# Kernel optimization log

Hardware: AMD Instinct MI355X
Metric: run time of the kernel (lower is better)

Reference implementation:

```python
import jax, jax.numpy as jnp
import numpy as np

B, N, F, D, H = 4, 2048, 128, 64, 4
NEG = -1000000000.0


def setup_inputs() -> dict:
    key = jax.random.key(0)
    k1, k2, k3, k4 = jax.random.split(key, 4)
    X = jax.random.normal(k1, (B, N, F), dtype=jnp.float32)
    A = jax.random.randint(k2, (N, N), 0, 2, dtype=jnp.int32)
    kernels = jax.random.normal(k3, (H, F, D), dtype=jnp.float32) * 0.1
    attn_kernels = jax.random.normal(k4, (H, D), dtype=jnp.float32) * 0.1
    return {"X": X, "A": A, "kernels": kernels, "attn_kernels": attn_kernels}


def reference(X, A, kernels, attn_kernels):
    # h: per-head linear projection  [H,B,N,D]
    h = jnp.einsum('bnf,hfd->hbnd', X, kernels)
    # per-node scalar scores e_i = h @ a  [H,B,N]
    s = jnp.einsum('hbnd,hd->hbn', h, attn_kernels)
    # pairwise additive score e_ij = relu(s_i + s_j)  [H,B,N,N]
    e = jax.nn.relu(s[:, :, :, None] + s[:, :, None, :])
    e = jnp.where(A[None, None, :, :] > 0, e, NEG)
    alpha = jax.nn.softmax(e, axis=-1)
    # dropout is identity at inference
    h_prime = jnp.einsum('hbnm,hbmd->hbnd', alpha, h)
    out = jnp.mean(h_prime, axis=0)           # mean over heads -> [B,N,D]
    return jax.nn.leaky_relu(out, negative_slope=0.2)
```

## Files before the change

### kernel.cpp

```cpp
#include <hip/hip_runtime.h>
#include <hip/hip_bf16.h>

typedef __attribute__((ext_vector_type(8))) short short8;
typedef __attribute__((ext_vector_type(4))) float f32x4;
typedef unsigned short u16;
typedef unsigned int u32;

constexpr int CB = 4, CN = 2048, CF = 128, CD = 64, CH = 4;
constexpr int IT = 32;

__device__ inline u32 fmap(float f) {
    u32 b = __float_as_uint(f);
    return b ^ ((u32)(((int)b) >> 31) | 0x80000000u);
}
__device__ inline float funmap(u32 u) {
    u32 b = (u & 0x80000000u) ? (u ^ 0x80000000u) : ~u;
    return __uint_as_float(b);
}
__device__ inline u16 bf16bits(float v) {
    __hip_bfloat16 b = __float2bfloat16(v);
    return *reinterpret_cast<u16*>(&b);
}

__global__ __launch_bounds__(256) void prep_k(const int* __restrict__ A,
                                              const float* __restrict__ W,
                                              u32* __restrict__ mask,
                                              u32* __restrict__ smax_u,
                                              u16* __restrict__ WThi,
                                              u16* __restrict__ WTlo) {
    int blk = blockIdx.x, t = threadIdx.x;
    if (blk < 16384) {
        int gid = blk * 256 + t;
        if (blk == 0 && t < CH * CB) smax_u[t] = 0u;
        unsigned long long mk = __ballot(A[gid] > 0);
        if ((t & 63) == 0) {
            mask[gid >> 5] = (u32)mk;
            mask[(gid >> 5) + 1] = (u32)(mk >> 32);
        }
    } else {
        int idx = (blk - 16384) * 256 + t;
        int h = idx >> 13;
        int f = (idx >> 6) & 127;
        int d = idx & 63;
        float v = W[idx];
        __hip_bfloat16 bh = __float2bfloat16(v);
        float lo = v - __bfloat162float(bh);
        int o = (h * CD + d) * CF + f;
        WThi[o] = *reinterpret_cast<u16*>(&bh);
        WTlo[o] = bf16bits(lo);
    }
}

__global__ __launch_bounds__(256, 2) void proj_k(const float* __restrict__ X,
                                                 const u16* __restrict__ WThi,
                                                 const u16* __restrict__ WTlo,
                                                 const float* __restrict__ AK,
                                                 u16* __restrict__ hT,
                                                 float* __restrict__ sout,
                                                 float* __restrict__ eout,
                                                 u32* __restrict__ smax_u) {
    __shared__ float tr[4][CD][17];

    int blk = blockIdx.x;
    int ntile = blk & 127;
    int b = blk >> 7;
    int n0 = ntile * 16;
    int t = threadIdx.x;
    int w = t >> 6, l = t & 63;
    int h = w;
    int row_l = l & 15, jg = l >> 4;

    const float* xrow = X + ((size_t)b * CN + n0 + row_l) * CF + jg * 8;
    const u16* whi = WThi + (size_t)h * CD * CF;
    const u16* wlo = WTlo + (size_t)h * CD * CF;

    float4 xa[4], xb[4];
#pragma unroll
    for (int kk = 0; kk < 4; ++kk) {
        xa[kk] = *reinterpret_cast<const float4*>(xrow + kk * 32);
        xb[kk] = *reinterpret_cast<const float4*>(xrow + kk * 32 + 4);
    }
    short8 bhi[4][4], blo[4][4];
#pragma unroll
    for (int kk = 0; kk < 4; ++kk)
#pragma unroll
        for (int dt = 0; dt < 4; ++dt) {
            int off = (dt * 16 + row_l) * CF + kk * 32 + jg * 8;
            bhi[kk][dt] = *reinterpret_cast<const short8*>(whi + off);
            blo[kk][dt] = *reinterpret_cast<const short8*>(wlo + off);
        }

    f32x4 c[4];
    f32x4 zero = {0.f, 0.f, 0.f, 0.f};
#pragma unroll
    for (int dt = 0; dt < 4; ++dt) c[dt] = zero;

#pragma unroll
    for (int kk = 0; kk < 4; ++kk) {
        float xv[8] = {xa[kk].x, xa[kk].y, xa[kk].z, xa[kk].w,
                       xb[kk].x, xb[kk].y, xb[kk].z, xb[kk].w};
        short8 ahi, alo;
#pragma unroll
        for (int e = 0; e < 8; ++e) {
            __hip_bfloat16 bh = __float2bfloat16(xv[e]);
            ahi[e] = (short)*reinterpret_cast<u16*>(&bh);
            alo[e] = (short)bf16bits(xv[e] - __bfloat162float(bh));
        }
#pragma unroll
        for (int dt = 0; dt < 4; ++dt) {
            c[dt] = __builtin_amdgcn_mfma_f32_16x16x32_bf16(ahi, bhi[kk][dt], c[dt], 0, 0, 0);
            c[dt] = __builtin_amdgcn_mfma_f32_16x16x32_bf16(ahi, blo[kk][dt], c[dt], 0, 0, 0);
            c[dt] = __builtin_amdgcn_mfma_f32_16x16x32_bf16(alo, bhi[kk][dt], c[dt], 0, 0, 0);
        }
    }

    float av[4];
#pragma unroll
    for (int dt = 0; dt < 4; ++dt) av[dt] = AK[h * CD + dt * 16 + row_l];
    float sacc[4];
#pragma unroll
    for (int r = 0; r < 4; ++r)
        sacc[r] = c[0][r] * av[0] + c[1][r] * av[1] + c[2][r] * av[2] + c[3][r] * av[3];
#pragma unroll
    for (int off = 1; off <= 8; off <<= 1)
#pragma unroll
        for (int r = 0; r < 4; ++r) sacc[r] += __shfl_xor(sacc[r], off, 64);

    float mx = fmaxf(fmaxf(sacc[0], sacc[1]), fmaxf(sacc[2], sacc[3]));
    mx = fmaxf(mx, __shfl_xor(mx, 16, 64));
    mx = fmaxf(mx, __shfl_xor(mx, 32, 64));
    if (l == 0) atomicMax(&smax_u[h * CB + b], fmap(mx));

    if (row_l == 0) {
#pragma unroll
        for (int r = 0; r < 4; ++r) {
            size_t si = (size_t)(h * CB + b) * CN + n0 + jg * 4 + r;
            sout[si] = sacc[r];
            eout[si] = __expf(sacc[r]);
        }
    }

#pragma unroll
    for (int dt = 0; dt < 4; ++dt)
#pragma unroll
        for (int r = 0; r < 4; ++r) tr[w][dt * 16 + row_l][jg * 4 + r] = c[dt][r];
    __syncthreads();

    short8* hTs = reinterpret_cast<short8*>(hT);
    int jc = l >> 5, d0 = l & 31;
#pragma unroll
    for (int half = 0; half < 2; ++half) {
        short8 pk;
#pragma unroll
        for (int e = 0; e < 8; ++e)
            pk[e] = (short)bf16bits(tr[w][half * 32 + d0][jc * 8 + e]);
        hTs[((size_t)(h * CB + b) * 256 + ntile * 2 + jc) * 64 + half * 32 + d0] = pk;
    }
}

__global__ __launch_bounds__(1024, 4) void attn_k(const u16* __restrict__ hT,
                                                  const float* __restrict__ s_ws,
                                                  const float* __restrict__ e_ws,
                                                  const u32* __restrict__ smax_u,
                                                  const u32* __restrict__ mask32,
                                                  float* __restrict__ out) {
    __shared__ alignas(16) float e_sl[CH][CN];
    __shared__ u32 m_lds[IT][65];
    __shared__ float cbuf[CH][2][IT][68];
    __shared__ float lbuf[CH][4][IT];

    int orig = blockIdx.x;
    int xcd = orig & 7, pos = orig >> 3;
    int b = xcd >> 1;
    int it = (xcd & 1) * 32 + pos;
    int i0 = it * IT;
    int t = threadIdx.x, w = t >> 6, l = t & 63;
    int hq = w >> 2, jq = w & 3;
    int row_l = l & 15, jg = l >> 4;

    for (int idx = t; idx < CH * CN; idx += 1024) {
        int hh = idx >> 11, j = idx & 2047;
        e_sl[hh][j] = e_ws[(size_t)(hh * CB + b) * CN + j];
    }
    for (int idx = t; idx < IT * 64; idx += 1024) {
        int r = idx >> 6, wd = idx & 63;
        m_lds[r][wd] = mask32[(size_t)(i0 + r) * 64 + wd];
    }
    __syncthreads();

    float smax = funmap(smax_u[hq * CB + b]);
    float si0 = s_ws[(size_t)(hq * CB + b) * CN + i0 + row_l];
    float si1 = s_ws[(size_t)(hq * CB + b) * CN + i0 + 16 + row_l];
    float m0 = fmaxf(si0 + smax, 0.f), m1 = fmaxf(si1 + smax, 0.f);
    float Ei0 = __expf(si0 - m0), Ci0 = __expf(-m0);
    float Ei1 = __expf(si1 - m1), Ci1 = __expf(-m1);

    f32x4 c0[4], c1[4], cl0, cl1;
    f32x4 zero = {0.f, 0.f, 0.f, 0.f};
#pragma unroll
    for (int dt = 0; dt < 4; ++dt) { c0[dt] = zero; c1[dt] = zero; }
    cl0 = zero; cl1 = zero;

    short8 ones;
#pragma unroll
    for (int e = 0; e < 8; ++e) ones[e] = (short)0x3F80;

    const short8* hp = reinterpret_cast<const short8*>(hT) +
                       ((size_t)(hq * CB + b) * 256 + jq * 64 + jg) * 64 + row_l;

    short8 bfA[4], bfB[4];
#pragma unroll
    for (int dt = 0; dt < 4; ++dt) bfA[dt] = hp[dt * 16];

#define ATTN_STEP(KK, BCUR, BNXT, KNXT)                                          \
    do {                                                                         \
        _Pragma("unroll") for (int dt = 0; dt < 4; ++dt)                         \
            BNXT[dt] = hp[(KNXT) * 256 + dt * 16];                               \
        int jl = jq * 512 + (KK) * 32 + jg * 8;                                  \
        f32x4 ej0 = *reinterpret_cast<const f32x4*>(&e_sl[hq][jl]);              \
        f32x4 ej1 = *reinterpret_cast<const f32x4*>(&e_sl[hq][jl + 4]);          \
        u32 by0 = m_lds[row_l][jq * 16 + (KK)] >> (jg * 8);                      \
        u32 by1 = m_lds[16 + row_l][jq * 16 + (KK)] >> (jg * 8);                 \
        short8 af0, af1;                                                         \
        _Pragma("unroll") for (int e = 0; e < 8; ++e) {                          \
            float ejv = (e < 4) ? ej0[e] : ej1[e - 4];                           \
            float w0 = ((by0 >> e) & 1u) ? fmaxf(Ei0 * ejv, Ci0) : 0.f;          \
            float w1 = ((by1 >> e) & 1u) ? fmaxf(Ei1 * ejv, Ci1) : 0.f;          \
            af0[e] = (short)bf16bits(w0);                                        \
            af1[e] = (short)bf16bits(w1);                                        \
        }                                                                        \
        _Pragma("unroll") for (int dt = 0; dt < 4; ++dt) {                       \
            c0[dt] = __builtin_amdgcn_mfma_f32_16x16x32_bf16(af0, BCUR[dt], c0[dt], 0, 0, 0); \
            c1[dt] = __builtin_amdgcn_mfma_f32_16x16x32_bf16(af1, BCUR[dt], c1[dt], 0, 0, 0); \
        }                                                                        \
        cl0 = __builtin_amdgcn_mfma_f32_16x16x32_bf16(af0, ones, cl0, 0, 0, 0);  \
        cl1 = __builtin_amdgcn_mfma_f32_16x16x32_bf16(af1, ones, cl1, 0, 0, 0);  \
    } while (0)

#pragma unroll
    for (int kp = 0; kp < 8; ++kp) {
        ATTN_STEP(2 * kp, bfA, bfB, 2 * kp + 1);
        ATTN_STEP(2 * kp + 1, bfB, bfA, (2 * kp + 2 < 16) ? 2 * kp + 2 : 15);
    }
#undef ATTN_STEP

    int slot = jq & 1;
    if (row_l == 0)
#pragma unroll
        for (int r = 0; r < 4; ++r) {
            lbuf[hq][jq][jg * 4 + r] = cl0[r];
            lbuf[hq][jq][16 + jg * 4 + r] = cl1[r];
        }
    if (jq < 2) {
#pragma unroll
        for (int dt = 0; dt < 4; ++dt)
#pragma unroll
            for (int r = 0; r < 4; ++r) {
                cbuf[hq][slot][jg * 4 + r][dt * 16 + row_l] = c0[dt][r];
                cbuf[hq][slot][16 + jg * 4 + r][dt * 16 + row_l] = c1[dt][r];
            }
    }
    __syncthreads();
    if (jq >= 2) {
#pragma unroll
        for (int dt = 0; dt < 4; ++dt)
#pragma unroll
            for (int r = 0; r < 4; ++r) {
                cbuf[hq][slot][jg * 4 + r][dt * 16 + row_l] += c0[dt][r];
                cbuf[hq][slot][16 + jg * 4 + r][dt * 16 + row_l] += c1[dt][r];
            }
    }
    __syncthreads();

    for (int idx = t; idx < IT * CD; idx += 1024) {
        int row = idx >> 6, d = idx & 63;
        float acc = 0.f;
#pragma unroll
        for (int h = 0; h < CH; ++h) {
            float num = cbuf[h][0][row][d] + cbuf[h][1][row][d];
            float den = lbuf[h][0][row] + lbuf[h][1][row] + lbuf[h][2][row] + lbuf[h][3][row];
            acc += num / fmaxf(den, 1e-30f);
        }
        float o = acc * 0.25f;
        out[((size_t)b * CN + i0 + row) * CD + d] = o > 0.f ? o : 0.2f * o;
    }
}

extern "C" void kernel_launch(void* const* d_in, const int* in_sizes, int n_in,
                              void* d_out, int out_size, void* d_ws, size_t ws_size,
                              hipStream_t stream) {
    const float* X  = (const float*)d_in[0];
    const int*   A  = (const int*)d_in[1];
    const float* W  = (const float*)d_in[2];
    const float* AK = (const float*)d_in[3];
    float* out = (float*)d_out;

    char* w = (char*)d_ws;
    float* s_ws = (float*)w;    w += 131072;
    float* e_ws = (float*)w;    w += 131072;
    u32* smax_ws = (u32*)w;     w += 256;
    u32* mask_ws = (u32*)w;     w += 524288;
    u16* hT = (u16*)w;          w += 4194304;
    u16* WThi = (u16*)w;        w += 65536;
    u16* WTlo = (u16*)w;        w += 65536;

    prep_k<<<16384 + 128, 256, 0, stream>>>(A, W, mask_ws, smax_ws, WThi, WTlo);
    proj_k<<<CB * (CN / 16), 256, 0, stream>>>(X, WThi, WTlo, AK, hT, s_ws, e_ws, smax_ws);
    attn_k<<<CB * (CN / IT), 1024, 0, stream>>>(hT, s_ws, e_ws, smax_ws, mask_ws, out);
}
```

Before: 68.85 us.

## Pre-swizzle weight fragments for coalesced loads, add MFMA priority, roll attention loop

The prep kernel now writes the bf16 hi/lo weight copies in the exact per-lane MFMA fragment order, so the projection kernel loads each short8 fragment contiguously across lanes instead of with strided gathers. The attention inner step raises wave priority around the MFMA block with s_setprio so matrix work is issued ahead of the other waves' scalar and conversion work. The attention k-loop is changed from fully unrolled to unroll 1, which cuts code size and register pressure but adds loop overhead and may limit cross-iteration scheduling.

```diff
diff --git a/kernel.cpp b/kernel.cpp
--- a/kernel.cpp
+++ b/kernel.cpp
@@ -39,15 +39,17 @@
         }
     } else {
         int idx = (blk - 16384) * 256 + t;
+        int e = idx & 7;
+        int l = (idx >> 3) & 63;
+        int dt = (idx >> 9) & 3;
+        int kk = (idx >> 11) & 3;
         int h = idx >> 13;
-        int f = (idx >> 6) & 127;
-        int d = idx & 63;
-        float v = W[idx];
+        int f = kk * 32 + (l >> 4) * 8 + e;
+        int d = dt * 16 + (l & 15);
+        float v = W[(h * CF + f) * CD + d];
         __hip_bfloat16 bh = __float2bfloat16(v);
-        float lo = v - __bfloat162float(bh);
-        int o = (h * CD + d) * CF + f;
-        WThi[o] = *reinterpret_cast<u16*>(&bh);
-        WTlo[o] = bf16bits(lo);
+        WThi[idx] = *reinterpret_cast<u16*>(&bh);
+        WTlo[idx] = bf16bits(v - __bfloat162float(bh));
     }
 }
 
@@ -71,8 +73,8 @@
     int row_l = l & 15, jg = l >> 4;
 
     const float* xrow = X + ((size_t)b * CN + n0 + row_l) * CF + jg * 8;
-    const u16* whi = WThi + (size_t)h * CD * CF;
-    const u16* wlo = WTlo + (size_t)h * CD * CF;
+    const short8* whiU = reinterpret_cast<const short8*>(WThi) + (size_t)h * 1024 + l;
+    const short8* wloU = reinterpret_cast<const short8*>(WTlo) + (size_t)h * 1024 + l;
 
     float4 xa[4], xb[4];
 #pragma unroll
@@ -85,9 +87,8 @@
     for (int kk = 0; kk < 4; ++kk)
 #pragma unroll
         for (int dt = 0; dt < 4; ++dt) {
-            int off = (dt * 16 + row_l) * CF + kk * 32 + jg * 8;
-            bhi[kk][dt] = *reinterpret_cast<const short8*>(whi + off);
-            blo[kk][dt] = *reinterpret_cast<const short8*>(wlo + off);
+            bhi[kk][dt] = whiU[(kk * 4 + dt) * 64];
+            blo[kk][dt] = wloU[(kk * 4 + dt) * 64];
         }
 
     f32x4 c[4];
@@ -229,18 +230,21 @@
             af0[e] = (short)bf16bits(w0);                                        \
             af1[e] = (short)bf16bits(w1);                                        \
         }                                                                        \
+        __builtin_amdgcn_s_setprio(1);                                           \
         _Pragma("unroll") for (int dt = 0; dt < 4; ++dt) {                       \
             c0[dt] = __builtin_amdgcn_mfma_f32_16x16x32_bf16(af0, BCUR[dt], c0[dt], 0, 0, 0); \
             c1[dt] = __builtin_amdgcn_mfma_f32_16x16x32_bf16(af1, BCUR[dt], c1[dt], 0, 0, 0); \
         }                                                                        \
         cl0 = __builtin_amdgcn_mfma_f32_16x16x32_bf16(af0, ones, cl0, 0, 0, 0);  \
         cl1 = __builtin_amdgcn_mfma_f32_16x16x32_bf16(af1, ones, cl1, 0, 0, 0);  \
+        __builtin_amdgcn_s_setprio(0);                                           \
     } while (0)
 
-#pragma unroll
-    for (int kp = 0; kp < 8; ++kp) {
-        ATTN_STEP(2 * kp, bfA, bfB, 2 * kp + 1);
-        ATTN_STEP(2 * kp + 1, bfB, bfA, (2 * kp + 2 < 16) ? 2 * kp + 2 : 15);
+#pragma unroll 1
+    for (int kp = 0; kp < 16; kp += 2) {
+        ATTN_STEP(kp, bfA, bfB, kp + 1);
+        int kn = (kp + 2 < 16) ? kp + 2 : 15;
+        ATTN_STEP(kp + 1, bfB, bfA, kn);
     }
 #undef ATTN_STEP
 
@@ -295,14 +299,14 @@
     const float* AK = (const float*)d_in[3];
     float* out = (float*)d_out;
 
-    char* w = (char*)d_ws;
-    float* s_ws = (float*)w;    w += 131072;
-    float* e_ws = (float*)w;    w += 131072;
-    u32* smax_ws = (u32*)w;     w += 256;
-    u32* mask_ws = (u32*)w;     w += 524288;
-    u16* hT = (u16*)w;          w += 4194304;
-    u16* WThi = (u16*)w;        w += 65536;
-    u16* WTlo = (u16*)w;        w += 65536;
+    char* wp = (char*)d_ws;
+    float* s_ws = (float*)wp;    wp += 131072;
+    float* e_ws = (float*)wp;    wp += 131072;
+    u32* smax_ws = (u32*)wp;     wp += 256;
+    u32* mask_ws = (u32*)wp;     wp += 524288;
+    u16* hT = (u16*)wp;          wp += 4194304;
+    u16* WThi = (u16*)wp;        wp += 65536;
+    u16* WTlo = (u16*)wp;        wp += 65536;
 
     prep_k<<<16384 + 128, 256, 0, stream>>>(A, W, mask_ws, smax_ws, WThi, WTlo);
     proj_k<<<CB * (CN / 16), 256, 0, stream>>>(X, WThi, WTlo, AK, hT, s_ws, e_ws, smax_ws);
```

Measured after the change: 61.80 us. 10.2% less time.
